# Optimization experiments

Measured on AMD Instinct MI355X. Metric: run time of the kernel, lower is better.

Reference implementation:

```python
import jax, jax.numpy as jnp
import numpy as np
from jax import lax

B, S, H = 64, 512, 768
L = 20          # num_labels
MAX_SPANS = 8   # span_number_classifier has MAX_SPANS+1 outputs


def setup_inputs() -> dict:
    key = jax.random.key(0)
    k = jax.random.split(key, 8)
    w = lambda i, shape: jax.random.normal(k[i], shape, jnp.float32) * 0.02
    return {
        "tokens_rep": jax.random.normal(k[0], (B, S, H), jnp.float32),
        "seq_rep": jax.random.normal(k[1], (B, H), jnp.float32),
        "w_start": w(2, (H,)), "b_start": jnp.zeros((), jnp.float32),
        "w_end": w(3, (H,)), "b_end": jnp.zeros((), jnp.float32),
        "W_nspans": w(4, (H, MAX_SPANS + 1)), "b_nspans": jnp.zeros((MAX_SPANS + 1,), jnp.float32),
        "W_span": w(5, (H, L)), "b_span": jnp.zeros((L,), jnp.float32),
        "W_pol": w(6, (H + L, L)), "b_pol": jnp.zeros((L,), jnp.float32),
    }


def _select_spans(ss, es, n_spans):
    """Faithful port of get_top_spans_nongreedy's while-loop.
    ss/es: [MAX_SPANS] ascending-sorted top indices (sentinel S beyond n_spans).
    Each iteration advances s_idx and/or e_idx, so 2*MAX_SPANS steps suffice."""
    def body(i, st):
        s_idx, e_idx, last_end, rem, out_s, out_e, cnt = st
        active = (rem > 0) & (s_idx < n_spans) & (e_idx < n_spans)
        s = ss[jnp.minimum(s_idx, MAX_SPANS - 1)]
        e = es[jnp.minimum(e_idx, MAX_SPANS - 1)]
        accept = active & (e > s) & (s >= last_end)
        inc_e = active & (~accept) & (e <= s)
        inc_s = active & (~accept) & (e > s)
        out_s = jnp.where(accept, out_s.at[cnt].set(s), out_s)
        out_e = jnp.where(accept, out_e.at[cnt].set(e), out_e)
        last_end = jnp.where(accept, e, last_end)
        a = accept.astype(jnp.int32)
        return (s_idx + a + inc_s.astype(jnp.int32),
                e_idx + a + inc_e.astype(jnp.int32),
                last_end, rem - a, out_s, out_e, cnt + a)

    z = jnp.zeros((MAX_SPANS,), jnp.int32)
    init = (jnp.int32(0), jnp.int32(0), jnp.int32(0), n_spans, z, z, jnp.int32(0))
    st = lax.fori_loop(0, 2 * MAX_SPANS, body, init)
    return st[4], st[5], st[6]  # starts, ends, count


def _per_item(tokens, starts, ends, fsl, n_spans, W_span, b_span):
    # sigmoid is monotone, so top-k of sigmoid(logits) == top-k of logits
    _, i_s = lax.top_k(starts, MAX_SPANS)
    _, i_e = lax.top_k(ends, MAX_SPANS)
    rank = jnp.arange(MAX_SPANS)
    keep = rank < n_spans
    ss = jnp.sort(jnp.where(keep, i_s, S).astype(jnp.int32))  # sentinel S sorts last
    es = jnp.sort(jnp.where(keep, i_e, S).astype(jnp.int32))
    out_s, out_e, cnt = _select_spans(ss, es, n_spans)
    valid = rank < cnt
    vf = valid.astype(tokens.dtype)

    # span mean-pooling tokens[s:e+1].mean(0) via a [MAX_SPANS,S] mask matmul
    t = jnp.arange(S)
    span_mask = ((t[None, :] >= out_s[:, None]) & (t[None, :] <= out_e[:, None])).astype(tokens.dtype)
    lengths = (out_e - out_s + 1).astype(tokens.dtype)
    span_vecs = (span_mask @ tokens) / lengths[:, None]         # [MAX_SPANS, H]

    mls = jax.nn.softmax(span_vecs @ W_span + b_span, axis=1)   # [MAX_SPANS, L]
    span_labels = jnp.argmax(mls, axis=1)
    fsl_soft = jax.nn.softmax(fsl)
    has_valid = cnt > 0

    labels_oh_m = jnp.zeros((L,), tokens.dtype).at[span_labels].max(vf)
    labels_oh_m = jnp.where(has_valid, labels_oh_m,
                            jnp.zeros((L,), tokens.dtype).at[jnp.argmax(fsl_soft)].set(1.0))
    spans_m = jnp.max(jnp.where(valid[:, None], mls, -jnp.inf), axis=0)
    spans_m = jnp.where(has_valid, spans_m, jnp.zeros((L,), tokens.dtype))
    starts_oh_m = jnp.zeros((S,), tokens.dtype).at[out_s].max(vf)
    ends_oh_m = jnp.zeros((S,), tokens.dtype).at[out_e].max(vf)

    # n_spans <= 1 branch
    labels_oh_1 = jnp.zeros((L,), tokens.dtype).at[jnp.argmax(fsl_soft)].set(1.0)
    starts_oh_1 = jnp.zeros((S,), tokens.dtype).at[jnp.argmax(starts)].set(1.0)
    ends_oh_1 = jnp.zeros((S,), tokens.dtype).at[jnp.argmax(ends)].set(1.0)

    single = n_spans <= 1
    spans = jnp.where(single, fsl_soft, spans_m)
    labels_oh = jnp.where(single, labels_oh_1, labels_oh_m)
    starts_oh = jnp.where(single, starts_oh_1, starts_oh_m)
    ends_oh = jnp.where(single, ends_oh_1, ends_oh_m)
    return spans, starts_oh, ends_oh, labels_oh


def reference(tokens_rep, seq_rep, w_start, b_start, w_end, b_end,
              W_nspans, b_nspans, W_span, b_span, W_pol, b_pol):
    full_seq_logits = seq_rep @ W_span + b_span        # [B, L]
    start_logits = tokens_rep @ w_start + b_start      # [B, S]
    end_logits = tokens_rep @ w_end + b_end            # [B, S]
    n_spans_logits = seq_rep @ W_nspans + b_nspans     # [B, MAX_SPANS+1]
    all_n_spans = jnp.argmax(n_spans_logits, axis=1).astype(jnp.int32)

    spans, starts_oh, ends_oh, labels_oh = jax.vmap(
        _per_item, in_axes=(0, 0, 0, 0, 0, None, None)
    )(tokens_rep, start_logits, end_logits, full_seq_logits, all_n_spans, W_span, b_span)

    pol_logits = jnp.concatenate([seq_rep, spans], axis=1) @ W_pol + b_pol
    return (start_logits, end_logits, spans, n_spans_logits, pol_logits,
            starts_oh, ends_oh, labels_oh)
```

## Files before the change

kernel.cpp:

```cpp
#include <hip/hip_runtime.h>
#include <math.h>

#define NB 64
#define SS 512
#define HH 768
#define LL 20
#define MS 8
#define NSPC 9

#define OFF_START 0
#define OFF_END   (NB*SS)
#define OFF_SPANS (2*NB*SS)
#define OFF_NSP   (2*NB*SS + NB*LL)
#define OFF_POL   (2*NB*SS + NB*LL + NB*NSPC)
#define OFF_SOH   (2*NB*SS + 2*NB*LL + NB*NSPC)
#define OFF_EOH   (3*NB*SS + 2*NB*LL + NB*NSPC)
#define OFF_LOH   (4*NB*SS + 2*NB*LL + NB*NSPC)

struct WS {
  float fsl[NB][LL];
  float mls[NB][MS][LL];
  int   nspans[NB];
  int   fslarg[NB];
  int   cnt[NB];
  int   out_s[NB][MS];
  int   out_e[NB][MS];
  int   slabel[NB][MS];
  float candSV[NB][16][MS];
  int   candSI[NB][16][MS];
  float candEV[NB][16][MS];
  int   candEI[NB][16][MS];
};

__global__ __launch_bounds__(256) void kA(
    const float4* __restrict__ tok,
    const float* __restrict__ wstart, const float* __restrict__ bstart,
    const float* __restrict__ wend,  const float* __restrict__ bend,
    const float* __restrict__ seq,
    const float* __restrict__ Wspan, const float* __restrict__ bspan,
    const float* __restrict__ Wnsp,  const float* __restrict__ bnsp,
    float* __restrict__ out, WS* __restrict__ ws)
{
  int t = threadIdx.x;
  int wave = t >> 6, lane = t & 63;

  if (blockIdx.x < 1024) {
    int b = blockIdx.x >> 4;
    int blk = blockIdx.x & 15;
    __shared__ float4 shs[HH/4], she[HH/4];
    __shared__ float lvS[32], lvE[32];
    const float4* wsg = (const float4*)wstart;
    const float4* weg = (const float4*)wend;
    for (int i = t; i < HH/4; i += 256) { shs[i] = wsg[i]; she[i] = weg[i]; }
    __syncthreads();
    int r0 = blockIdx.x * 32 + wave * 8;
    const float4* base = tok + (size_t)r0 * (HH/4);
    float as[8] = {0.f,0.f,0.f,0.f,0.f,0.f,0.f,0.f};
    float ae[8] = {0.f,0.f,0.f,0.f,0.f,0.f,0.f,0.f};
    #pragma unroll
    for (int k = 0; k < 3; ++k) {
      int idx = k*64 + lane;
      float4 a = shs[idx], c = she[idx];
      #pragma unroll
      for (int j = 0; j < 8; ++j) {
        float4 x = base[(size_t)j * (HH/4) + idx];
        as[j] += x.x*a.x + x.y*a.y + x.z*a.z + x.w*a.w;
        ae[j] += x.x*c.x + x.y*c.y + x.z*c.z + x.w*c.w;
      }
    }
    float b0 = bstart[0], b1 = bend[0];
    #pragma unroll
    for (int j = 0; j < 8; ++j) {
      float a = as[j], e = ae[j];
      for (int off = 32; off >= 1; off >>= 1) { a += __shfl_down(a, off); e += __shfl_down(e, off); }
      if (lane == 0) {
        out[OFF_START + r0 + j] = a + b0;
        out[OFF_END   + r0 + j] = e + b1;
        int slot = wave*8 + j;
        lvS[slot] = a + b0; lvE[slot] = e + b1;
      }
    }
    __syncthreads();
    if (wave < 2) {
      float v = -INFINITY; int idx = 0x7fffffff;
      if (lane < 32) {
        v = wave ? lvE[lane] : lvS[lane];
        idx = blk*32 + lane;
      }
      int rank = 0;
      #pragma unroll
      for (int j = 0; j < 32; ++j) {
        float vj = __shfl(v, j); int ij = __shfl(idx, j);
        if (vj > v || (vj == v && ij < idx)) ++rank;
      }
      if (lane < 32 && rank < MS) {
        if (wave == 0) { ws->candSV[b][blk][rank] = v; ws->candSI[b][blk][rank] = idx; }
        else           { ws->candEV[b][blk][rank] = v; ws->candEI[b][blk][rank] = idx; }
      }
    }
  } else {
    int b = blockIdx.x - 1024;
    __shared__ float sh[HH];
    __shared__ float logits[LL + NSPC];
    for (int i = t; i < HH; i += 256) sh[i] = seq[b*HH + i];
    __syncthreads();
    for (int o = wave; o < LL + NSPC; o += 4) {
      float acc = 0.f;
      if (o < LL) {
        for (int k = 0; k < HH/64; ++k) { int h = lane + 64*k; acc += sh[h] * Wspan[h*LL + o]; }
      } else {
        int j = o - LL;
        for (int k = 0; k < HH/64; ++k) { int h = lane + 64*k; acc += sh[h] * Wnsp[h*NSPC + j]; }
      }
      for (int off = 32; off >= 1; off >>= 1) acc += __shfl_down(acc, off);
      if (lane == 0) logits[o] = acc + (o < LL ? bspan[o] : bnsp[o - LL]);
    }
    __syncthreads();
    if (t == 0) {
      int bi = 0; float bv = logits[LL];
      #pragma unroll
      for (int j = 1; j < NSPC; ++j) { float v = logits[LL + j]; if (v > bv) { bv = v; bi = j; } }
      ws->nspans[b] = bi;
      int fi = 0; float fv = logits[0];
      #pragma unroll
      for (int j = 1; j < LL; ++j) { float v = logits[j]; if (v > fv) { fv = v; fi = j; } }
      ws->fslarg[b] = fi;
    }
    if (t < LL)  ws->fsl[b][t] = logits[t];
    if (t < NSPC) out[OFF_NSP + b*NSPC + t] = logits[LL + t];
  }
}

__global__ __launch_bounds__(256) void kB(
    float* __restrict__ out, WS* __restrict__ ws)
{
  int b = blockIdx.x;
  int t = threadIdx.x;
  int wave = t >> 6, lane = t & 63;

  __shared__ int topI[2][MS];
  __shared__ int sh_cnt, sh_single;
  __shared__ int sh_os[MS], sh_oe[MS];

  if (wave < 2) {
    const float* cv = wave ? &ws->candEV[b][0][0] : &ws->candSV[b][0][0];
    const int*   ci = wave ? &ws->candEI[b][0][0] : &ws->candSI[b][0][0];
    float c0v = cv[lane], c1v = cv[lane + 64];
    int   c0i = ci[lane], c1i = ci[lane + 64];
    #pragma unroll
    for (int k = 0; k < MS; ++k) {
      float lv = c0v; int li = c0i;
      if (c1v > lv || (c1v == lv && c1i < li)) { lv = c1v; li = c1i; }
      #pragma unroll
      for (int m = 32; m >= 1; m >>= 1) {
        float ov = __shfl_xor(lv, m); int oi = __shfl_xor(li, m);
        if (ov > lv || (ov == lv && oi < li)) { lv = ov; li = oi; }
      }
      if (lane == 0) topI[wave][k] = li;
      if (c0i == li) c0v = -INFINITY;
      if (c1i == li) c1v = -INFINITY;
    }
  }
  __syncthreads();

  if (wave == 0) {
    int n = ws->nspans[b];
    int xs = SS, xe = SS;
    if (lane < MS && lane < n) { xs = topI[0][lane]; xe = topI[1][lane]; }
    int rs = 0, re = 0;
    #pragma unroll
    for (int j = 0; j < MS; ++j) {
      int xj = __shfl(xs, j);
      if (xj < xs || (xj == xs && j < lane)) ++rs;
      int yj = __shfl(xe, j);
      if (yj < xe || (yj == xe && j < lane)) ++re;
    }
    int ss_srt = 0, es_srt = 0;
    #pragma unroll
    for (int j = 0; j < MS; ++j) {
      int xj = __shfl(xs, j); int rj = __shfl(rs, j);
      if (rj == lane) ss_srt = xj;
      int yj = __shfl(xe, j); int qj = __shfl(re, j);
      if (qj == lane) es_srt = yj;
    }
    int si = 0, ei = 0, last = 0, rem = n, cnt = 0;
    int my_os = 0, my_oe = 0;
    for (int it = 0; it < 2*MS; ++it) {
      bool active = (rem > 0) && (si < n) && (ei < n);
      int s = __shfl(ss_srt, si < MS ? si : MS - 1);
      int e = __shfl(es_srt, ei < MS ? ei : MS - 1);
      bool accept = active && (e > s) && (s >= last);
      bool ince = active && !accept && (e <= s);
      bool incs = active && !accept && (e > s);
      if (accept) {
        if (lane == cnt) { my_os = s; my_oe = e; }
        last = e; ++cnt; --rem; ++si; ++ei;
      } else {
        si += incs ? 1 : 0; ei += ince ? 1 : 0;
      }
    }
    if (lane < MS) {
      sh_os[lane] = my_os; sh_oe[lane] = my_oe;
      ws->out_s[b][lane] = my_os; ws->out_e[b][lane] = my_oe;
    }
    if (lane == 0) {
      sh_cnt = cnt; sh_single = (ws->nspans[b] <= 1) ? 1 : 0;
      ws->cnt[b] = cnt;
    }
  }
  __syncthreads();

  int cnt = sh_cnt, single = sh_single;
  #pragma unroll
  for (int pp = 0; pp < 2; ++pp) {
    int pos = t + pp * 256;
    float sval = 0.f, eval = 0.f;
    if (single) {
      if (pos == topI[0][0]) sval = 1.f;
      if (pos == topI[1][0]) eval = 1.f;
    } else {
      for (int i = 0; i < cnt; ++i) {
        if (pos == sh_os[i]) sval = 1.f;
        if (pos == sh_oe[i]) eval = 1.f;
      }
    }
    out[OFF_SOH + b*SS + pos] = sval;
    out[OFF_EOH + b*SS + pos] = eval;
  }
}

__global__ __launch_bounds__(1024) void kC(
    const float4* __restrict__ tok,
    const float* __restrict__ Wspan, const float* __restrict__ bspan,
    WS* __restrict__ ws)
{
  int b = blockIdx.x >> 3;
  int i = blockIdx.x & (MS - 1);
  if (i >= ws->cnt[b]) return;
  int s0 = ws->out_s[b][i], e0 = ws->out_e[b][i];
  int t = threadIdx.x;
  int g = t >> 8;
  int tid = t & 255;

  __shared__ float4 part[4][HH/4];
  __shared__ float pooled[HH];
  __shared__ float lg[LL];

  if (tid < HH/4) {
    float4 acc = make_float4(0.f, 0.f, 0.f, 0.f);
    const float4* base = tok + (size_t)b * SS * (HH/4) + tid;
    #pragma unroll 4
    for (int r = s0 + g; r <= e0; r += 4) {
      float4 x = base[(size_t)r * (HH/4)];
      acc.x += x.x; acc.y += x.y; acc.z += x.z; acc.w += x.w;
    }
    part[g][tid] = acc;
  }
  __syncthreads();

  if (t < HH/4) {
    float4 p0 = part[0][t], p1 = part[1][t], p2 = part[2][t], p3 = part[3][t];
    float inv = 1.f / (float)(e0 - s0 + 1);
    float4 s;
    s.x = (p0.x + p1.x + p2.x + p3.x) * inv;
    s.y = (p0.y + p1.y + p2.y + p3.y) * inv;
    s.z = (p0.z + p1.z + p2.z + p3.z) * inv;
    s.w = (p0.w + p1.w + p2.w + p3.w) * inv;
    ((float4*)pooled)[t] = s;
  }
  __syncthreads();

  int wave = t >> 6, lane = t & 63;
  for (int l = wave; l < LL; l += 16) {
    float acc = 0.f;
    for (int k = 0; k < HH/64; ++k) { int h = lane + 64*k; acc += pooled[h] * Wspan[h*LL + l]; }
    for (int off = 32; off >= 1; off >>= 1) acc += __shfl_down(acc, off);
    if (lane == 0) lg[l] = acc + bspan[l];
  }
  __syncthreads();

  if (t == 0) {
    float v[LL]; float mx = -INFINITY;
    #pragma unroll
    for (int l = 0; l < LL; ++l) { v[l] = lg[l]; mx = fmaxf(mx, v[l]); }
    int am = 0; float av = v[0];
    #pragma unroll
    for (int l = 1; l < LL; ++l) if (v[l] > av) { av = v[l]; am = l; }
    float sum = 0.f;
    #pragma unroll
    for (int l = 0; l < LL; ++l) { v[l] = expf(v[l] - mx); sum += v[l]; }
    float isum = 1.f / sum;
    #pragma unroll
    for (int l = 0; l < LL; ++l) ws->mls[b][i][l] = v[l] * isum;
    ws->slabel[b][i] = am;
  }
}

__global__ __launch_bounds__(256) void kD(
    const float* __restrict__ seq,
    const float* __restrict__ Wpol, const float* __restrict__ bpol,
    float* __restrict__ out, WS* __restrict__ ws)
{
  int b = blockIdx.x;
  int t = threadIdx.x;
  __shared__ float sp[LL];
  __shared__ float fsl_soft[LL];
  int n = ws->nspans[b];
  int single = (n <= 1) ? 1 : 0;
  int cnt = ws->cnt[b];
  int fa = ws->fslarg[b];
  if (t == 0) {
    float lg[LL]; float mx = -INFINITY;
    #pragma unroll
    for (int l = 0; l < LL; ++l) { lg[l] = ws->fsl[b][l]; mx = fmaxf(mx, lg[l]); }
    float sum = 0.f;
    #pragma unroll
    for (int l = 0; l < LL; ++l) { lg[l] = expf(lg[l] - mx); sum += lg[l]; }
    float isum = 1.f / sum;
    #pragma unroll
    for (int l = 0; l < LL; ++l) fsl_soft[l] = lg[l] * isum;
  }
  __syncthreads();
  if (t < LL) {
    float v;
    if (single) v = fsl_soft[t];
    else if (cnt > 0) { v = -INFINITY; for (int i = 0; i < cnt; ++i) v = fmaxf(v, ws->mls[b][i][t]); }
    else v = 0.f;
    sp[t] = v;
    out[OFF_SPANS + b*LL + t] = v;
    float lo = 0.f;
    if (single || cnt == 0) lo = (t == fa) ? 1.f : 0.f;
    else { for (int i = 0; i < cnt; ++i) if (ws->slabel[b][i] == t) lo = 1.f; }
    out[OFF_LOH + b*LL + t] = lo;
  }
  __syncthreads();
  int wave = t >> 6, lane = t & 63;
  const float* seqb = seq + b*HH;
  for (int l = wave; l < LL; l += 4) {
    float acc = 0.f;
    for (int k = 0; k < 13; ++k) {
      int h = lane + 64*k;
      if (h < HH + LL) {
        float v = (h < HH) ? seqb[h] : sp[h - HH];
        acc += v * Wpol[h*LL + l];
      }
    }
    for (int off = 32; off >= 1; off >>= 1) acc += __shfl_down(acc, off);
    if (lane == 0) out[OFF_POL + b*LL + l] = acc + bpol[l];
  }
}

extern "C" void kernel_launch(void* const* d_in, const int* in_sizes, int n_in,
                              void* d_out, int out_size, void* d_ws, size_t ws_size,
                              hipStream_t stream)
{
  const float* tok    = (const float*)d_in[0];
  const float* seq    = (const float*)d_in[1];
  const float* wstart = (const float*)d_in[2];
  const float* bstart = (const float*)d_in[3];
  const float* wend   = (const float*)d_in[4];
  const float* bend   = (const float*)d_in[5];
  const float* Wnsp   = (const float*)d_in[6];
  const float* bnsp   = (const float*)d_in[7];
  const float* Wspan  = (const float*)d_in[8];
  const float* bspan  = (const float*)d_in[9];
  const float* Wpol   = (const float*)d_in[10];
  const float* bpol   = (const float*)d_in[11];
  float* out = (float*)d_out;
  WS* ws = (WS*)d_ws;

  kA<<<1088, 256, 0, stream>>>((const float4*)tok, wstart, bstart, wend, bend,
                               seq, Wspan, bspan, Wnsp, bnsp, out, ws);
  kB<<<NB, 256, 0, stream>>>(out, ws);
  kC<<<NB*MS, 1024, 0, stream>>>((const float4*)tok, Wspan, bspan, ws);
  kD<<<NB, 256, 0, stream>>>(seq, Wpol, bpol, out, ws);
}
```

Baseline: 79.58 us.

## Fuse span selection kernel into span pooling kernel, redundantly per span block

The span-selection kernel is merged into the pooling kernel. Each of the 8 blocks per batch item recomputes the top-k merge and greedy span selection in shared memory, then pools its own span. The one-hot outputs and the count are written only by block 0. This removes one kernel launch and the workspace round trip for span indices, at the cost of doing the selection work 8 times over.

```diff
diff --git a/kernel.cpp b/kernel.cpp
--- a/kernel.cpp
+++ b/kernel.cpp
@@ -23,8 +23,6 @@
   int   nspans[NB];
   int   fslarg[NB];
   int   cnt[NB];
-  int   out_s[NB][MS];
-  int   out_e[NB][MS];
   int   slabel[NB][MS];
   float candSV[NB][16][MS];
   int   candSI[NB][16][MS];
@@ -131,10 +129,13 @@
   }
 }
 
-__global__ __launch_bounds__(256) void kB(
+__global__ __launch_bounds__(1024) void kC(
+    const float4* __restrict__ tok,
+    const float* __restrict__ Wspan, const float* __restrict__ bspan,
     float* __restrict__ out, WS* __restrict__ ws)
 {
-  int b = blockIdx.x;
+  int b = blockIdx.x >> 3;
+  int i = blockIdx.x & (MS - 1);
   int t = threadIdx.x;
   int wave = t >> 6, lane = t & 63;
 
@@ -199,49 +200,37 @@
         si += incs ? 1 : 0; ei += ince ? 1 : 0;
       }
     }
-    if (lane < MS) {
-      sh_os[lane] = my_os; sh_oe[lane] = my_oe;
-      ws->out_s[b][lane] = my_os; ws->out_e[b][lane] = my_oe;
-    }
-    if (lane == 0) {
-      sh_cnt = cnt; sh_single = (ws->nspans[b] <= 1) ? 1 : 0;
-      ws->cnt[b] = cnt;
-    }
+    if (lane < MS) { sh_os[lane] = my_os; sh_oe[lane] = my_oe; }
+    if (lane == 0) { sh_cnt = cnt; sh_single = (n <= 1) ? 1 : 0; }
   }
   __syncthreads();
 
   int cnt = sh_cnt, single = sh_single;
-  #pragma unroll
-  for (int pp = 0; pp < 2; ++pp) {
-    int pos = t + pp * 256;
-    float sval = 0.f, eval = 0.f;
-    if (single) {
-      if (pos == topI[0][0]) sval = 1.f;
-      if (pos == topI[1][0]) eval = 1.f;
-    } else {
-      for (int i = 0; i < cnt; ++i) {
-        if (pos == sh_os[i]) sval = 1.f;
-        if (pos == sh_oe[i]) eval = 1.f;
-      }
-    }
-    out[OFF_SOH + b*SS + pos] = sval;
-    out[OFF_EOH + b*SS + pos] = eval;
-  }
-}
-
-__global__ __launch_bounds__(1024) void kC(
-    const float4* __restrict__ tok,
-    const float* __restrict__ Wspan, const float* __restrict__ bspan,
-    WS* __restrict__ ws)
-{
-  int b = blockIdx.x >> 3;
-  int i = blockIdx.x & (MS - 1);
-  if (i >= ws->cnt[b]) return;
-  int s0 = ws->out_s[b][i], e0 = ws->out_e[b][i];
-  int t = threadIdx.x;
+
+  if (i == 0) {
+    if (t < SS) {
+      int pos = t;
+      float sval = 0.f, eval = 0.f;
+      if (single) {
+        if (pos == topI[0][0]) sval = 1.f;
+        if (pos == topI[1][0]) eval = 1.f;
+      } else {
+        for (int k = 0; k < cnt; ++k) {
+          if (pos == sh_os[k]) sval = 1.f;
+          if (pos == sh_oe[k]) eval = 1.f;
+        }
+      }
+      out[OFF_SOH + b*SS + pos] = sval;
+      out[OFF_EOH + b*SS + pos] = eval;
+    }
+    if (t == 0) ws->cnt[b] = cnt;
+  }
+
+  if (i >= cnt) return;
+  int s0 = sh_os[i], e0 = sh_oe[i];
+
   int g = t >> 8;
   int tid = t & 255;
-
   __shared__ float4 part[4][HH/4];
   __shared__ float pooled[HH];
   __shared__ float lg[LL];
@@ -270,7 +259,6 @@
   }
   __syncthreads();
 
-  int wave = t >> 6, lane = t & 63;
   for (int l = wave; l < LL; l += 16) {
     float acc = 0.f;
     for (int k = 0; k < HH/64; ++k) { int h = lane + 64*k; acc += pooled[h] * Wspan[h*LL + l]; }
@@ -371,7 +359,6 @@
 
   kA<<<1088, 256, 0, stream>>>((const float4*)tok, wstart, bstart, wend, bend,
                                seq, Wspan, bspan, Wnsp, bnsp, out, ws);
-  kB<<<NB, 256, 0, stream>>>(out, ws);
-  kC<<<NB*MS, 1024, 0, stream>>>((const float4*)tok, Wspan, bspan, ws);
+  kC<<<NB*MS, 1024, 0, stream>>>((const float4*)tok, Wspan, bspan, out, ws);
   kD<<<NB, 256, 0, stream>>>(seq, Wpol, bpol, out, ws);
 }
```

Measured after the change: 77.20 us. 3.0% less time.
